# Kernel optimization log

Measured on AMD Instinct MI355X. Metric: run time of the kernel, lower is better.

Reference implementation:

```python
import jax, jax.numpy as jnp
import numpy as np

B, C, H, W = 64, 64, 64, 64
KD = 64  # kernel_dim == res == dim (required by the torch reshapes)


def _ln(t, g, b, eps=1e-5):
    mu = jnp.mean(t, axis=-1, keepdims=True)
    var = jnp.var(t, axis=-1, keepdims=True)
    return (t - mu) * jax.lax.rsqrt(var + eps) * g + b


def _cos_map(n, kd):
    i = jnp.arange(n, dtype=jnp.float32)[:, None]
    j = jnp.arange(kd, dtype=jnp.float32)[None, :]
    return jnp.cos(i * j * jnp.pi / n) / kd


def setup_inputs() -> dict:
    key = jax.random.key(0)
    ks = jax.random.split(key, 6)
    s = 0.02
    return {
        "x": jax.random.normal(ks[0], (B, C, H, W), jnp.float32),
        "freq_embed": jax.random.normal(ks[1], (H, W, C), jnp.float32),
        "g_k": jnp.ones((C,), jnp.float32), "b_k": jnp.zeros((C,), jnp.float32),
        "Wk": jax.random.normal(ks[2], (C, KD), jnp.float32) * s, "bk": jnp.zeros((KD,), jnp.float32),
        "g_z": jnp.ones((C,), jnp.float32), "b_z": jnp.zeros((C,), jnp.float32),
        "Wz": jax.random.normal(ks[3], (C, C), jnp.float32) * s, "bz": jnp.zeros((C,), jnp.float32),
        "g_o": jnp.ones((KD,), jnp.float32), "b_o": jnp.zeros((KD,), jnp.float32),
        "Wo": jax.random.normal(ks[4], (KD, C), jnp.float32) * s, "bo": jnp.zeros((C,), jnp.float32),
    }


def reference(x, freq_embed, g_k, b_k, Wk, bk, g_z, b_z, Wz, bz, g_o, b_o, Wo, bo):
    # x: (B,C,H,W) -> (B,H,W,C), matching the torch permute branch
    x = jnp.transpose(x, (0, 2, 3, 1))
    Bc, Hc, Wc, Cc = x.shape
    kd = Wk.shape[1]
    xin = x + freq_embed[None]                    # freq_embed broadcast over batch
    k = _ln(xin, g_k, b_k) @ Wk + bk              # (B,H,W,kd)
    z = _ln(freq_embed, g_z, b_z) @ Wz + bz       # to_k(freq_embed): (H,W,C)
    cosn = _cos_map(Hc, kd)                       # (H,kd)
    cosm = _cos_map(Wc, kd)                       # (W,kd)
    i = jnp.arange(Hc, dtype=jnp.float32)[:, None]
    j = jnp.arange(Wc, dtype=jnp.float32)[None, :]
    decay = (jnp.exp(-(i + j) / max(Hc, Wc)) / kd).astype(x.dtype)  # (H,W)
    wexp = decay[:, :, None] ** z                 # (H,W,C), decay > 0
    # separable forward DCT (two kernel-1 conv1d == two contractions)
    t = jnp.einsum('nh,bhwc->bnwc', cosn, k)
    t = jnp.einsum('mw,bnwc->bnmc', cosm, t)
    t = t * wexp[None]                            # exponential-decay spectral gate
    # separable inverse DCT
    t = jnp.einsum('nh,bnmc->bhmc', cosn, t)
    t = jnp.einsum('mw,bhmc->bhwc', cosm, t)
    out = _ln(t, g_o, b_o) * jax.nn.silu(z)[None]
    out = out @ Wo + bo
    return jnp.transpose(out, (0, 3, 1, 2))       # back to BCHW
```

## Files before the change

kernel.cpp:

```cpp
#include <hip/hip_runtime.h>


typedef __attribute__((ext_vector_type(8))) short short8;
typedef __attribute__((ext_vector_type(4))) float f32x4;
typedef __attribute__((ext_vector_type(4))) unsigned short us4;

__device__ __forceinline__ unsigned short bfhi(float f) {
    return (unsigned short)(__builtin_bit_cast(unsigned int, f) >> 16);
}
__device__ __forceinline__ float hif(float f) {
    return __builtin_bit_cast(float, __builtin_bit_cast(unsigned int, f) & 0xFFFF0000u);
}
__device__ __forceinline__ int swa(int row, int col) {
    return (row << 7) + (((col >> 3) ^ (row & 7)) << 4) + ((col & 7) << 1);
}
__device__ __forceinline__ short8 fragrd(const short* buf, int row, int kc) {
    int a = (row << 7) + ((kc ^ (row & 7)) << 4);
    return *(const short8*)((const char*)buf + a);
}
__device__ __forceinline__ f32x4 mm3(short8 ah, short8 al, short8 bh, short8 bl, f32x4 acc) {
    acc = __builtin_amdgcn_mfma_f32_16x16x32_bf16(ah, bh, acc, 0, 0, 0);
    acc = __builtin_amdgcn_mfma_f32_16x16x32_bf16(ah, bl, acc, 0, 0, 0);
    acc = __builtin_amdgcn_mfma_f32_16x16x32_bf16(al, bh, acc, 0, 0, 0);
    return acc;
}

__device__ __forceinline__ void mm_block(const short* Ah, const short* Al,
                                         const short* Bh, const short* Bl,
                                         int m0, int n0, int l15, int q,
                                         f32x4 (&acc)[2][2]) {
    const f32x4 zero = {0.f, 0.f, 0.f, 0.f};
    acc[0][0] = zero; acc[0][1] = zero; acc[1][0] = zero; acc[1][1] = zero;
    #pragma unroll
    for (int kb = 0; kb < 2; ++kb) {
        int kc = (kb << 2) + q;
        short8 a0h = fragrd(Ah, m0 + l15, kc);
        short8 a0l = fragrd(Al, m0 + l15, kc);
        short8 a1h = fragrd(Ah, m0 + 16 + l15, kc);
        short8 a1l = fragrd(Al, m0 + 16 + l15, kc);
        short8 b0h = fragrd(Bh, n0 + l15, kc);
        short8 b0l = fragrd(Bl, n0 + l15, kc);
        short8 b1h = fragrd(Bh, n0 + 16 + l15, kc);
        short8 b1l = fragrd(Bl, n0 + 16 + l15, kc);
        acc[0][0] = mm3(a0h, a0l, b0h, b0l, acc[0][0]);
        acc[0][1] = mm3(a0h, a0l, b1h, b1l, acc[0][1]);
        acc[1][0] = mm3(a1h, a1l, b0h, b0l, acc[1][0]);
        acc[1][1] = mm3(a1h, a1l, b1h, b1l, acc[1][1]);
    }
}

__device__ __forceinline__ void mm_block_regB(const short* Ah, const short* Al,
                                              const short8 (&bf)[2][2][2],
                                              int m0, int l15, int q,
                                              f32x4 (&acc)[2][2]) {
    const f32x4 zero = {0.f, 0.f, 0.f, 0.f};
    acc[0][0] = zero; acc[0][1] = zero; acc[1][0] = zero; acc[1][1] = zero;
    #pragma unroll
    for (int kb = 0; kb < 2; ++kb) {
        int kc = (kb << 2) + q;
        short8 a0h = fragrd(Ah, m0 + l15, kc);
        short8 a0l = fragrd(Al, m0 + l15, kc);
        short8 a1h = fragrd(Ah, m0 + 16 + l15, kc);
        short8 a1l = fragrd(Al, m0 + 16 + l15, kc);
        #pragma unroll
        for (int u = 0; u < 2; ++u) {
            acc[0][u] = mm3(a0h, a0l, bf[u][kb][0], bf[u][kb][1], acc[0][u]);
            acc[1][u] = mm3(a1h, a1l, bf[u][kb][0], bf[u][kb][1], acc[1][u]);
        }
    }
}

__global__ __launch_bounds__(256) void k_pre1(
    const float* __restrict__ g_k, const float* __restrict__ b_k,
    const float* __restrict__ Wk, const float* __restrict__ bk,
    const float* __restrict__ g_z, const float* __restrict__ b_z,
    const float* __restrict__ Wz, const float* __restrict__ bz,
    const float* __restrict__ Wo,
    unsigned short* __restrict__ WkTh, unsigned short* __restrict__ WkTl,
    float* __restrict__ su_k, float* __restrict__ v_k,
    unsigned short* __restrict__ WzTh, unsigned short* __restrict__ WzTl,
    float* __restrict__ su_z, float* __restrict__ v_z,
    unsigned short* __restrict__ WoTh, unsigned short* __restrict__ WoTl,
    unsigned short* __restrict__ cos_hi, unsigned short* __restrict__ cos_lo) {
    int t = threadIdx.x;
    if (blockIdx.x < 16) {
        int n = blockIdx.x * 4 + (t >> 6);
        int c = t & 63;
        float wk = Wk[c * 64 + n];
        float a = g_k[c] * wk;
        WkTh[n * 64 + c] = bfhi(a);
        WkTl[n * 64 + c] = bfhi(a - hif(a));
        float sa = a, sv = b_k[c] * wk;
        #pragma unroll
        for (int off = 32; off > 0; off >>= 1) {
            sa += __shfl_xor(sa, off, 64);
            sv += __shfl_xor(sv, off, 64);
        }
        if (c == 0) { su_k[n] = sa; v_k[n] = sv + bk[n]; }
        float wz = Wz[c * 64 + n];
        float az = g_z[c] * wz;
        WzTh[n * 64 + c] = bfhi(az);
        WzTl[n * 64 + c] = bfhi(az - hif(az));
        float saz = az, svz = b_z[c] * wz;
        #pragma unroll
        for (int off = 32; off > 0; off >>= 1) {
            saz += __shfl_xor(saz, off, 64);
            svz += __shfl_xor(svz, off, 64);
        }
        if (c == 0) { su_z[n] = saz; v_z[n] = svz + bz[n]; }
        float wo = Wo[c * 64 + n];
        WoTh[n * 64 + c] = bfhi(wo);
        WoTl[n * 64 + c] = bfhi(wo - hif(wo));
    } else {
        int idx = (blockIdx.x - 16) * 256 + t;
        int i = idx >> 6, j = idx & 63;
        float ang = (float)(i * j) * 3.14159265358979323846f * (1.0f / 64.0f);
        float v = cosf(ang) * (1.0f / 64.0f);
        cos_hi[idx] = bfhi(v);
        cos_lo[idx] = bfhi(v - hif(v));
    }
}

__global__ __launch_bounds__(256) void k_pre2(
    const float* __restrict__ freq,
    const unsigned short* __restrict__ WzTh_g, const unsigned short* __restrict__ WzTl_g,
    const float* __restrict__ su_z, const float* __restrict__ v_z,
    float* __restrict__ siluzT, float* __restrict__ wexpT,
    float* __restrict__ freqT) {
    __shared__ __align__(16) short Ah[4096], Al[4096], Bh[4096], Bl[4096];
    __shared__ float muS[64], rsS[64];
    __shared__ float tile[64][65];
    int t = threadIdx.x;
    if (blockIdx.x < 64) {
        int h = blockIdx.x;
        #pragma unroll
        for (int p = 0; p < 2; ++p) {
            int e = t + p * 256;
            int row = e >> 3, ch = e & 7;
            int a = (row << 7) + (((ch ^ (row & 7)) << 4));
            *(uint4*)((char*)Bh + a) = *(const uint4*)&WzTh_g[row * 64 + ch * 8];
            *(uint4*)((char*)Bl + a) = *(const uint4*)&WzTl_g[row * 64 + ch * 8];
        }
        int w = t >> 2, c0 = (t & 3) << 4;
        float4 fr[4];
        float s1 = 0.f, s2 = 0.f;
        #pragma unroll
        for (int i = 0; i < 4; ++i) {
            fr[i] = *(const float4*)&freq[(h * 64 + w) * 64 + c0 + 4 * i];
            s1 += fr[i].x + fr[i].y + fr[i].z + fr[i].w;
            s2 += fr[i].x * fr[i].x + fr[i].y * fr[i].y + fr[i].z * fr[i].z + fr[i].w * fr[i].w;
        }
        s1 += __shfl_xor(s1, 1, 64); s1 += __shfl_xor(s1, 2, 64);
        s2 += __shfl_xor(s2, 1, 64); s2 += __shfl_xor(s2, 2, 64);
        float mu = s1 * (1.0f / 64.0f);
        float var = s2 * (1.0f / 64.0f) - mu * mu;
        float rs = rsqrtf(var + 1e-5f);
        if ((t & 3) == 0) { muS[w] = mu; rsS[w] = rs; }
        const float* fp = (const float*)fr;
        #pragma unroll
        for (int i = 0; i < 4; ++i) {
            us4 hv, lv;
            #pragma unroll
            for (int r = 0; r < 4; ++r) {
                float f = fp[i * 4 + r];
                hv[r] = bfhi(f);
                lv[r] = bfhi(f - hif(f));
            }
            int a = swa(w, c0 + 4 * i);
            *(us4*)((char*)Ah + a) = hv;
            *(us4*)((char*)Al + a) = lv;
        }
        __syncthreads();
        int lane = t & 63, wv = t >> 6;
        int q = lane >> 4, l15 = lane & 15;
        int m0 = (wv & 1) << 5, n0 = (wv >> 1) << 5;
        f32x4 acc[2][2];
        mm_block(Ah, Al, Bh, Bl, m0, n0, l15, q, acc);
        #pragma unroll
        for (int u = 0; u < 2; ++u) {
            int c = n0 + (u << 4) + l15;
            float suc = su_z[c], vc = v_z[c];
            #pragma unroll
            for (int ti = 0; ti < 2; ++ti) {
                int wb = m0 + (ti << 4) + (q << 2);
                float4 mu4 = *(const float4*)&muS[wb];
                float4 rs4 = *(const float4*)&rsS[wb];
                float4 sil, wx;
                #pragma unroll
                for (int r = 0; r < 4; ++r) {
                    float z = ((const float*)&rs4)[r] * (acc[ti][u][r] - ((const float*)&mu4)[r] * suc) + vc;
                    float lnd = -(float)(h + wb + r) * 0.015625f - 4.1588830833596718565f;
                    ((float*)&sil)[r] = z / (1.0f + expf(-z));
                    ((float*)&wx)[r] = expf(z * lnd);
                }
                int base = (c * 64 + h) * 64 + wb;
                *(float4*)&siluzT[base] = sil;
                *(float4*)&wexpT[base] = wx;
            }
        }
    } else {
        int h = blockIdx.x - 64;
        int w = t >> 2, c0 = (t & 3) << 4;
        #pragma unroll
        for (int i = 0; i < 4; ++i)
            *(float4*)&tile[w][c0 + 4 * i] = *(const float4*)&freq[(h * 64 + w) * 64 + c0 + 4 * i];
        __syncthreads();
        int w0 = (t & 15) << 2;
        #pragma unroll
        for (int p = 0; p < 4; ++p) {
            int c = (t >> 4) + 16 * p;
            float4 fv = make_float4(tile[w0][c], tile[w0 + 1][c], tile[w0 + 2][c], tile[w0 + 3][c]);
            *(float4*)&freqT[(c * 64 + h) * 64 + w0] = fv;
        }
    }
}

__global__ __launch_bounds__(256, 4) void k_k(
    const float* __restrict__ x, const float* __restrict__ freqT,
    const unsigned short* __restrict__ WkTh_g, const unsigned short* __restrict__ WkTl_g,
    const float* __restrict__ su_k, const float* __restrict__ v_k,
    float* __restrict__ planes) {
    __shared__ __align__(16) short Ah[4096], Al[4096];
    __shared__ __align__(16) float red1[4][64], red2[4][64];
    __shared__ __align__(16) float muS[64], rsS[64];
    int b = blockIdx.x >> 6, h = blockIdx.x & 63;
    int t = threadIdx.x;
    int lane = t & 63, wv = t >> 6;
    int q = lane >> 4, l15 = lane & 15;
    int m0 = (wv & 1) << 5, n0 = (wv >> 1) << 5;
    short8 bf[2][2][2];
    #pragma unroll
    for (int u = 0; u < 2; ++u)
        #pragma unroll
        for (int kb = 0; kb < 2; ++kb) {
            int off = (n0 + (u << 4) + l15) * 64 + ((kb << 2) + q) * 8;
            bf[u][kb][0] = *(const short8*)&WkTh_g[off];
            bf[u][kb][1] = *(const short8*)&WkTl_g[off];
        }
    int g = t >> 4, w0 = (t & 15) << 2, c0 = g << 2;
    const float* xb = x + (size_t)b * 262144 + h * 64;
    float4 xv[4], fv[4];
    #pragma unroll
    for (int i = 0; i < 4; ++i) {
        xv[i] = *(const float4*)&xb[(c0 + i) * 4096 + w0];
        fv[i] = *(const float4*)&freqT[(c0 + i) * 4096 + h * 64 + w0];
    }
    float4 s1 = {0, 0, 0, 0}, s2 = {0, 0, 0, 0};
    #pragma unroll
    for (int i = 0; i < 4; ++i) {
        xv[i].x += fv[i].x; xv[i].y += fv[i].y; xv[i].z += fv[i].z; xv[i].w += fv[i].w;
        s1.x += xv[i].x; s1.y += xv[i].y; s1.z += xv[i].z; s1.w += xv[i].w;
        s2.x += xv[i].x * xv[i].x; s2.y += xv[i].y * xv[i].y;
        s2.z += xv[i].z * xv[i].z; s2.w += xv[i].w * xv[i].w;
    }
    const float* vp = (const float*)xv;
    #pragma unroll
    for (int j = 0; j < 4; ++j) {
        us4 hv, lv;
        #pragma unroll
        for (int r = 0; r < 4; ++r) {
            float f = vp[r * 4 + j];
            hv[r] = bfhi(f);
            lv[r] = bfhi(f - hif(f));
        }
        int a = swa(w0 + j, c0);
        *(us4*)((char*)Ah + a) = hv;
        *(us4*)((char*)Al + a) = lv;
    }
    #pragma unroll
    for (int r = 0; r < 4; ++r) {
        float a1 = ((const float*)&s1)[r];
        float a2 = ((const float*)&s2)[r];
        a1 += __shfl_xor(a1, 16, 64); a1 += __shfl_xor(a1, 32, 64);
        a2 += __shfl_xor(a2, 16, 64); a2 += __shfl_xor(a2, 32, 64);
        ((float*)&s1)[r] = a1;
        ((float*)&s2)[r] = a2;
    }
    if (lane < 16) {
        *(float4*)&red1[wv][lane << 2] = s1;
        *(float4*)&red2[wv][lane << 2] = s2;
    }
    __syncthreads();
    if (t < 64) {
        float a1 = red1[0][t] + red1[1][t] + red1[2][t] + red1[3][t];
        float a2 = red2[0][t] + red2[1][t] + red2[2][t] + red2[3][t];
        float mu = a1 * (1.0f / 64.0f);
        float var = a2 * (1.0f / 64.0f) - mu * mu;
        muS[t] = mu; rsS[t] = rsqrtf(var + 1e-5f);
    }
    __syncthreads();
    f32x4 acc[2][2];
    mm_block_regB(Ah, Al, bf, m0, l15, q, acc);
    #pragma unroll
    for (int u = 0; u < 2; ++u) {
        int n = n0 + (u << 4) + l15;
        float sun = su_k[n], vn = v_k[n];
        #pragma unroll
        for (int ti = 0; ti < 2; ++ti) {
            int wb = m0 + (ti << 4) + (q << 2);
            float4 mu4 = *(const float4*)&muS[wb];
            float4 rs4 = *(const float4*)&rsS[wb];
            float4 o;
            o.x = rs4.x * (acc[ti][u][0] - mu4.x * sun) + vn;
            o.y = rs4.y * (acc[ti][u][1] - mu4.y * sun) + vn;
            o.z = rs4.z * (acc[ti][u][2] - mu4.z * sun) + vn;
            o.w = rs4.w * (acc[ti][u][3] - mu4.w * sun) + vn;
            *(float4*)&planes[((size_t)(b * 64 + n) * 64 + h) * 64 + wb] = o;
        }
    }
}

__global__ __launch_bounds__(128, 2) void k_spec(
    float* __restrict__ planes,
    const unsigned short* __restrict__ cos_hi, const unsigned short* __restrict__ cos_lo,
    const float* __restrict__ wexpT) {
    __shared__ __align__(16) short DhS[2][4096], DlS[2][4096];
    int t = threadIdx.x;
    int wv = t >> 6, lane = t & 63;
    int q = lane >> 4, l15 = lane & 15;
    int pid = blockIdx.x * 2 + wv;
    int c = pid & 63;
    float* po = planes + (size_t)pid * 4096;
    const float* wx = wexpT + (size_t)c * 4096;
    short* dh = DhS[wv];
    short* dl = DlS[wv];

    short8 cf[4][2][2];
    #pragma unroll
    for (int rg = 0; rg < 4; ++rg)
        #pragma unroll
        for (int kb = 0; kb < 2; ++kb) {
            int off = (rg * 16 + l15) * 64 + ((kb << 2) + q) * 8;
            cf[rg][kb][0] = *(const short8*)&cos_hi[off];
            cf[rg][kb][1] = *(const short8*)&cos_lo[off];
        }

    #pragma unroll
    for (int jg = 0; jg < 16; ++jg) {
        float f0 = po[(jg * 4 + 0) * 64 + lane];
        float f1 = po[(jg * 4 + 1) * 64 + lane];
        float f2 = po[(jg * 4 + 2) * 64 + lane];
        float f3 = po[(jg * 4 + 3) * 64 + lane];
        us4 hv, lv;
        hv[0] = bfhi(f0); lv[0] = bfhi(f0 - hif(f0));
        hv[1] = bfhi(f1); lv[1] = bfhi(f1 - hif(f1));
        hv[2] = bfhi(f2); lv[2] = bfhi(f2 - hif(f2));
        hv[3] = bfhi(f3); lv[3] = bfhi(f3 - hif(f3));
        int a = swa(lane, jg << 2);
        *(us4*)((char*)dh + a) = hv;
        *(us4*)((char*)dl + a) = lv;
    }

    short8 af[4][2][2];
    f32x4 acc[2][2];
    const f32x4 zacc = {0.f, 0.f, 0.f, 0.f};

#define LOAD_AF()                                                            \
    _Pragma("unroll")                                                        \
    for (int rg = 0; rg < 4; ++rg) {                                         \
        _Pragma("unroll")                                                    \
        for (int kb = 0; kb < 2; ++kb) {                                     \
            af[rg][kb][0] = fragrd(dh, rg * 16 + l15, (kb << 2) + q);        \
            af[rg][kb][1] = fragrd(dl, rg * 16 + l15, (kb << 2) + q);        \
        }                                                                    \
    }

#define QMM(ASRC, BSRC)                                                      \
    acc[0][0] = zacc; acc[0][1] = zacc; acc[1][0] = zacc; acc[1][1] = zacc;  \
    __builtin_amdgcn_s_setprio(1);                                           \
    _Pragma("unroll")                                                        \
    for (int kb = 0; kb < 2; ++kb)                                           \
        _Pragma("unroll")                                                    \
        for (int ti = 0; ti < 2; ++ti)                                       \
            _Pragma("unroll")                                                \
            for (int u = 0; u < 2; ++u)                                      \
                acc[ti][u] = mm3(ASRC[2 * mq + ti][kb][0], ASRC[2 * mq + ti][kb][1], \
                                 BSRC[2 * nq + u][kb][0], BSRC[2 * nq + u][kb][1],   \
                                 acc[ti][u]);                                \
    __builtin_amdgcn_s_setprio(0);

#define WB_T()                                                               \
    _Pragma("unroll")                                                        \
    for (int ti = 0; ti < 2; ++ti)                                           \
        _Pragma("unroll")                                                    \
        for (int u = 0; u < 2; ++u) {                                        \
            int row = (nq << 5) + (u << 4) + l15;                            \
            int col = (mq << 5) + (ti << 4) + (q << 2);                      \
            int a = swa(row, col);                                           \
            us4 hv, lv;                                                      \
            _Pragma("unroll")                                                \
            for (int r = 0; r < 4; ++r) {                                    \
                float f = acc[ti][u][r];                                     \
                hv[r] = bfhi(f);                                             \
                lv[r] = bfhi(f - hif(f));                                    \
            }                                                                \
            *(us4*)((char*)dh + a) = hv;                                     \
            *(us4*)((char*)dl + a) = lv;                                     \
        }

    LOAD_AF()
    #pragma unroll
    for (int mq = 0; mq < 2; ++mq)
        #pragma unroll
        for (int nq = 0; nq < 2; ++nq) {
            QMM(af, cf)
            WB_T()
        }

    LOAD_AF()
    #pragma unroll
    for (int mq = 0; mq < 2; ++mq)
        #pragma unroll
        for (int nq = 0; nq < 2; ++nq) {
            float wxr[2][2][4];
            #pragma unroll
            for (int ti = 0; ti < 2; ++ti)
                #pragma unroll
                for (int u = 0; u < 2; ++u)
                    #pragma unroll
                    for (int r = 0; r < 4; ++r)
                        wxr[ti][u][r] = wx[((mq << 5) + (ti << 4) + (q << 2) + r) * 64
                                           + (nq << 5) + (u << 4) + l15];
            QMM(af, cf)
            #pragma unroll
            for (int ti = 0; ti < 2; ++ti)
                #pragma unroll
                for (int u = 0; u < 2; ++u)
                    #pragma unroll
                    for (int r = 0; r < 4; ++r)
                        acc[ti][u][r] *= wxr[ti][u][r];
            WB_T()
        }

    LOAD_AF()
    #pragma unroll
    for (int mq = 0; mq < 2; ++mq)
        #pragma unroll
        for (int nq = 0; nq < 2; ++nq) {
            QMM(cf, af)
            #pragma unroll
            for (int ti = 0; ti < 2; ++ti)
                #pragma unroll
                for (int u = 0; u < 2; ++u)
                    #pragma unroll
                    for (int r = 0; r < 4; ++r) {
                        int row = (mq << 5) + (ti << 4) + (q << 2) + r;
                        int col = (nq << 5) + (u << 4) + l15;
                        int a = swa(row, col);
                        float f = acc[ti][u][r];
                        *(unsigned short*)((char*)dh + a) = bfhi(f);
                        *(unsigned short*)((char*)dl + a) = bfhi(f - hif(f));
                    }
        }

    LOAD_AF()
    #pragma unroll
    for (int mq = 0; mq < 2; ++mq)
        #pragma unroll
        for (int nq = 0; nq < 2; ++nq) {
            QMM(af, cf)
            #pragma unroll
            for (int ti = 0; ti < 2; ++ti)
                #pragma unroll
                for (int u = 0; u < 2; ++u)
                    #pragma unroll
                    for (int r = 0; r < 4; ++r) {
                        int h = (mq << 5) + (ti << 4) + (q << 2) + r;
                        int w = (nq << 5) + (u << 4) + l15;
                        po[h * 64 + w] = acc[ti][u][r];
                    }
        }
#undef LOAD_AF
#undef QMM
#undef WB_T
}

__global__ __launch_bounds__(256, 4) void k_out(
    const float* __restrict__ planes, const float* __restrict__ siluzT,
    const float* __restrict__ g_o, const float* __restrict__ b_o,
    const unsigned short* __restrict__ WoTh_g, const unsigned short* __restrict__ WoTl_g,
    const float* __restrict__ bo, float* __restrict__ out) {
    __shared__ __align__(16) short Ah[4096], Al[4096];
    __shared__ __align__(16) float red1[4][64], red2[4][64];
    __shared__ __align__(16) float muS[64], rsS[64];
    int b = blockIdx.x >> 6, h = blockIdx.x & 63;
    int t = threadIdx.x;
    int lane = t & 63, wv = t >> 6;
    int q = lane >> 4, l15 = lane & 15;
    int m0 = (wv & 1) << 5, n0 = (wv >> 1) << 5;
    short8 bf[2][2][2];
    #pragma unroll
    for (int u = 0; u < 2; ++u)
        #pragma unroll
        for (int kb = 0; kb < 2; ++kb) {
            int off = (n0 + (u << 4) + l15) * 64 + ((kb << 2) + q) * 8;
            bf[u][kb][0] = *(const short8*)&WoTh_g[off];
            bf[u][kb][1] = *(const short8*)&WoTl_g[off];
        }
    int g = t >> 4, w0 = (t & 15) << 2, c0 = g << 2;
    const float* pb = planes + (size_t)b * 262144 + h * 64;
    float4 vr[4], szr[4];
    #pragma unroll
    for (int i = 0; i < 4; ++i) {
        vr[i] = *(const float4*)&pb[(c0 + i) * 4096 + w0];
        szr[i] = *(const float4*)&siluzT[(c0 + i) * 4096 + h * 64 + w0];
    }
    float4 s1 = {0, 0, 0, 0}, s2 = {0, 0, 0, 0};
    #pragma unroll
    for (int i = 0; i < 4; ++i) {
        s1.x += vr[i].x; s1.y += vr[i].y; s1.z += vr[i].z; s1.w += vr[i].w;
        s2.x += vr[i].x * vr[i].x; s2.y += vr[i].y * vr[i].y;
        s2.z += vr[i].z * vr[i].z; s2.w += vr[i].w * vr[i].w;
    }
    #pragma unroll
    for (int r = 0; r < 4; ++r) {
        float a1 = ((const float*)&s1)[r];
        float a2 = ((const float*)&s2)[r];
        a1 += __shfl_xor(a1, 16, 64); a1 += __shfl_xor(a1, 32, 64);
        a2 += __shfl_xor(a2, 16, 64); a2 += __shfl_xor(a2, 32, 64);
        ((float*)&s1)[r] = a1;
        ((float*)&s2)[r] = a2;
    }
    if (lane < 16) {
        *(float4*)&red1[wv][lane << 2] = s1;
        *(float4*)&red2[wv][lane << 2] = s2;
    }
    __syncthreads();
    if (t < 64) {
        float a1 = red1[0][t] + red1[1][t] + red1[2][t] + red1[3][t];
        float a2 = red2[0][t] + red2[1][t] + red2[2][t] + red2[3][t];
        float mu = a1 * (1.0f / 64.0f);
        float var = a2 * (1.0f / 64.0f) - mu * mu;
        muS[t] = mu; rsS[t] = rsqrtf(var + 1e-5f);
    }
    __syncthreads();
    {
        float4 mu4 = *(const float4*)&muS[w0];
        float4 rs4 = *(const float4*)&rsS[w0];
        #pragma unroll
        for (int i = 0; i < 4; ++i) {
            int cc = c0 + i;
            float go = g_o[cc], boc = b_o[cc];
            vr[i].x = ((vr[i].x - mu4.x) * rs4.x * go + boc) * szr[i].x;
            vr[i].y = ((vr[i].y - mu4.y) * rs4.y * go + boc) * szr[i].y;
            vr[i].z = ((vr[i].z - mu4.z) * rs4.z * go + boc) * szr[i].z;
            vr[i].w = ((vr[i].w - mu4.w) * rs4.w * go + boc) * szr[i].w;
        }
        const float* vp = (const float*)vr;
        #pragma unroll
        for (int j = 0; j < 4; ++j) {
            us4 hv, lv;
            #pragma unroll
            for (int r = 0; r < 4; ++r) {
                float f = vp[r * 4 + j];
                hv[r] = bfhi(f);
                lv[r] = bfhi(f - hif(f));
            }
            int a = swa(w0 + j, c0);
            *(us4*)((char*)Ah + a) = hv;
            *(us4*)((char*)Al + a) = lv;
        }
    }
    __syncthreads();
    f32x4 acc[2][2];
    mm_block_regB(Ah, Al, bf, m0, l15, q, acc);
    #pragma unroll
    for (int u = 0; u < 2; ++u) {
        int o_ = n0 + (u << 4) + l15;
        float bov = bo[o_];
        #pragma unroll
        for (int ti = 0; ti < 2; ++ti) {
            int wb = m0 + (ti << 4) + (q << 2);
            float4 o;
            o.x = acc[ti][u][0] + bov;
            o.y = acc[ti][u][1] + bov;
            o.z = acc[ti][u][2] + bov;
            o.w = acc[ti][u][3] + bov;
            *(float4*)&out[((size_t)(b * 64 + o_) * 64 + h) * 64 + wb] = o;
        }
    }
}

extern "C" void kernel_launch(void* const* d_in, const int* in_sizes, int n_in,
                              void* d_out, int out_size, void* d_ws, size_t ws_size,
                              hipStream_t stream) {
    const float* x    = (const float*)d_in[0];
    const float* freq = (const float*)d_in[1];
    const float* g_k  = (const float*)d_in[2];
    const float* b_k  = (const float*)d_in[3];
    const float* Wk   = (const float*)d_in[4];
    const float* bk   = (const float*)d_in[5];
    const float* g_z  = (const float*)d_in[6];
    const float* b_z  = (const float*)d_in[7];
    const float* Wz   = (const float*)d_in[8];
    const float* bz   = (const float*)d_in[9];
    const float* g_o  = (const float*)d_in[10];
    const float* b_o  = (const float*)d_in[11];
    const float* Wo   = (const float*)d_in[12];
    const float* bo   = (const float*)d_in[13];
    float* out = (float*)d_out;

    float* ws = (float*)d_ws;
    float* planes = ws;
    float* siluzT = planes + 16777216;
    float* wexpT  = siluzT + 262144;
    float* freqT  = wexpT + 262144;
    float* su_k   = freqT + 262144;
    float* v_k    = su_k + 64;
    float* su_z   = v_k + 64;
    float* v_z    = su_z + 64;
    unsigned short* cos_hi = (unsigned short*)(v_z + 64);
    unsigned short* cos_lo = cos_hi + 4096;
    unsigned short* WkTh = cos_lo + 4096;
    unsigned short* WkTl = WkTh + 4096;
    unsigned short* WzTh = WkTl + 4096;
    unsigned short* WzTl = WzTh + 4096;
    unsigned short* WoTh = WzTl + 4096;
    unsigned short* WoTl = WoTh + 4096;

    k_pre1<<<32, 256, 0, stream>>>(g_k, b_k, Wk, bk, g_z, b_z, Wz, bz, Wo,
                                   WkTh, WkTl, su_k, v_k, WzTh, WzTl, su_z, v_z,
                                   WoTh, WoTl, cos_hi, cos_lo);
    k_pre2<<<128, 256, 0, stream>>>(freq, WzTh, WzTl, su_z, v_z, siluzT, wexpT, freqT);
    k_k<<<4096, 256, 0, stream>>>(x, freqT, WkTh, WkTl, su_k, v_k, planes);
    k_spec<<<2048, 128, 0, stream>>>(planes, cos_hi, cos_lo, wexpT);
    k_out<<<4096, 256, 0, stream>>>(planes, siluzT, g_o, b_o, WoTh, WoTl, bo, out);
}
```

Before: 230.7 us.

## Process four rows per block in k_k/k_out with register prefetch and padded plane stride

Each block of k_k and k_out now handles four h rows instead of one. It double-buffers the shared A tiles and prefetches the next rows' global loads into registers while the current row's MFMA runs. The planes and transposed per-channel buffers get a padded stride (4160 instead of 4096), apparently to reduce channel/bank conflicts across planes. This cuts the grid size by four and amortises the weight-fragment loads, at the cost of more registers and shared memory, with launch bounds lowered to 3 blocks per CU.

```diff
diff --git a/kernel.cpp b/kernel.cpp
--- a/kernel.cpp
+++ b/kernel.cpp
@@ -1,5 +1,8 @@
 #include <hip/hip_runtime.h>
 
+
+#define PL_ST 4160
+#define TC_ST 4160
 
 typedef __attribute__((ext_vector_type(8))) short short8;
 typedef __attribute__((ext_vector_type(4))) float f32x4;
@@ -193,7 +196,7 @@
                     ((float*)&sil)[r] = z / (1.0f + expf(-z));
                     ((float*)&wx)[r] = expf(z * lnd);
                 }
-                int base = (c * 64 + h) * 64 + wb;
+                size_t base = (size_t)c * TC_ST + h * 64 + wb;
                 *(float4*)&siluzT[base] = sil;
                 *(float4*)&wexpT[base] = wx;
             }
@@ -210,20 +213,20 @@
         for (int p = 0; p < 4; ++p) {
             int c = (t >> 4) + 16 * p;
             float4 fv = make_float4(tile[w0][c], tile[w0 + 1][c], tile[w0 + 2][c], tile[w0 + 3][c]);
-            *(float4*)&freqT[(c * 64 + h) * 64 + w0] = fv;
-        }
-    }
-}
-
-__global__ __launch_bounds__(256, 4) void k_k(
+            *(float4*)&freqT[(size_t)c * TC_ST + h * 64 + w0] = fv;
+        }
+    }
+}
+
+__global__ __launch_bounds__(256, 3) void k_k(
     const float* __restrict__ x, const float* __restrict__ freqT,
     const unsigned short* __restrict__ WkTh_g, const unsigned short* __restrict__ WkTl_g,
     const float* __restrict__ su_k, const float* __restrict__ v_k,
     float* __restrict__ planes) {
-    __shared__ __align__(16) short Ah[4096], Al[4096];
+    __shared__ __align__(16) short Ah[2][4096], Al[2][4096];
     __shared__ __align__(16) float red1[4][64], red2[4][64];
-    __shared__ __align__(16) float muS[64], rsS[64];
-    int b = blockIdx.x >> 6, h = blockIdx.x & 63;
+    __shared__ float muS[64], rsS[64];
+    int b = blockIdx.x >> 4, h0 = (blockIdx.x & 15) << 2;
     int t = threadIdx.x;
     int lane = t & 63, wv = t >> 6;
     int q = lane >> 4, l15 = lane & 15;
@@ -238,74 +241,93 @@
             bf[u][kb][1] = *(const short8*)&WkTl_g[off];
         }
     int g = t >> 4, w0 = (t & 15) << 2, c0 = g << 2;
-    const float* xb = x + (size_t)b * 262144 + h * 64;
-    float4 xv[4], fv[4];
-    #pragma unroll
-    for (int i = 0; i < 4; ++i) {
-        xv[i] = *(const float4*)&xb[(c0 + i) * 4096 + w0];
-        fv[i] = *(const float4*)&freqT[(c0 + i) * 4096 + h * 64 + w0];
-    }
-    float4 s1 = {0, 0, 0, 0}, s2 = {0, 0, 0, 0};
-    #pragma unroll
-    for (int i = 0; i < 4; ++i) {
-        xv[i].x += fv[i].x; xv[i].y += fv[i].y; xv[i].z += fv[i].z; xv[i].w += fv[i].w;
-        s1.x += xv[i].x; s1.y += xv[i].y; s1.z += xv[i].z; s1.w += xv[i].w;
-        s2.x += xv[i].x * xv[i].x; s2.y += xv[i].y * xv[i].y;
-        s2.z += xv[i].z * xv[i].z; s2.w += xv[i].w * xv[i].w;
-    }
-    const float* vp = (const float*)xv;
-    #pragma unroll
-    for (int j = 0; j < 4; ++j) {
-        us4 hv, lv;
+    const float* xb = x + (size_t)b * 262144;
+    float4 xr[2][4], fr[2][4];
+    #pragma unroll
+    for (int pi = 0; pi < 2; ++pi) {
+        int h = h0 + pi;
+        #pragma unroll
+        for (int i = 0; i < 4; ++i) {
+            xr[pi][i] = *(const float4*)&xb[(c0 + i) * 4096 + h * 64 + w0];
+            fr[pi][i] = *(const float4*)&freqT[(size_t)(c0 + i) * TC_ST + h * 64 + w0];
+        }
+    }
+    #pragma unroll
+    for (int it = 0; it < 4; ++it) {
+        int s = it & 1;
+        int h = h0 + it;
+        float4 vv[4];
+        float4 s1 = {0, 0, 0, 0}, s2 = {0, 0, 0, 0};
+        #pragma unroll
+        for (int i = 0; i < 4; ++i) {
+            float4 a = xr[s][i], f = fr[s][i];
+            a.x += f.x; a.y += f.y; a.z += f.z; a.w += f.w;
+            vv[i] = a;
+            s1.x += a.x; s1.y += a.y; s1.z += a.z; s1.w += a.w;
+            s2.x += a.x * a.x; s2.y += a.y * a.y; s2.z += a.z * a.z; s2.w += a.w * a.w;
+        }
+        const float* vp = (const float*)vv;
+        #pragma unroll
+        for (int j = 0; j < 4; ++j) {
+            us4 hv, lv;
+            #pragma unroll
+            for (int r = 0; r < 4; ++r) {
+                float f = vp[r * 4 + j];
+                hv[r] = bfhi(f);
+                lv[r] = bfhi(f - hif(f));
+            }
+            int a = swa(w0 + j, c0);
+            *(us4*)((char*)Ah[s] + a) = hv;
+            *(us4*)((char*)Al[s] + a) = lv;
+        }
         #pragma unroll
         for (int r = 0; r < 4; ++r) {
-            float f = vp[r * 4 + j];
-            hv[r] = bfhi(f);
-            lv[r] = bfhi(f - hif(f));
-        }
-        int a = swa(w0 + j, c0);
-        *(us4*)((char*)Ah + a) = hv;
-        *(us4*)((char*)Al + a) = lv;
-    }
-    #pragma unroll
-    for (int r = 0; r < 4; ++r) {
-        float a1 = ((const float*)&s1)[r];
-        float a2 = ((const float*)&s2)[r];
-        a1 += __shfl_xor(a1, 16, 64); a1 += __shfl_xor(a1, 32, 64);
-        a2 += __shfl_xor(a2, 16, 64); a2 += __shfl_xor(a2, 32, 64);
-        ((float*)&s1)[r] = a1;
-        ((float*)&s2)[r] = a2;
-    }
-    if (lane < 16) {
-        *(float4*)&red1[wv][lane << 2] = s1;
-        *(float4*)&red2[wv][lane << 2] = s2;
-    }
-    __syncthreads();
-    if (t < 64) {
-        float a1 = red1[0][t] + red1[1][t] + red1[2][t] + red1[3][t];
-        float a2 = red2[0][t] + red2[1][t] + red2[2][t] + red2[3][t];
-        float mu = a1 * (1.0f / 64.0f);
-        float var = a2 * (1.0f / 64.0f) - mu * mu;
-        muS[t] = mu; rsS[t] = rsqrtf(var + 1e-5f);
-    }
-    __syncthreads();
-    f32x4 acc[2][2];
-    mm_block_regB(Ah, Al, bf, m0, l15, q, acc);
-    #pragma unroll
-    for (int u = 0; u < 2; ++u) {
-        int n = n0 + (u << 4) + l15;
-        float sun = su_k[n], vn = v_k[n];
-        #pragma unroll
-        for (int ti = 0; ti < 2; ++ti) {
-            int wb = m0 + (ti << 4) + (q << 2);
-            float4 mu4 = *(const float4*)&muS[wb];
-            float4 rs4 = *(const float4*)&rsS[wb];
-            float4 o;
-            o.x = rs4.x * (acc[ti][u][0] - mu4.x * sun) + vn;
-            o.y = rs4.y * (acc[ti][u][1] - mu4.y * sun) + vn;
-            o.z = rs4.z * (acc[ti][u][2] - mu4.z * sun) + vn;
-            o.w = rs4.w * (acc[ti][u][3] - mu4.w * sun) + vn;
-            *(float4*)&planes[((size_t)(b * 64 + n) * 64 + h) * 64 + wb] = o;
+            float a1 = ((const float*)&s1)[r];
+            float a2 = ((const float*)&s2)[r];
+            a1 += __shfl_xor(a1, 16, 64); a1 += __shfl_xor(a1, 32, 64);
+            a2 += __shfl_xor(a2, 16, 64); a2 += __shfl_xor(a2, 32, 64);
+            ((float*)&s1)[r] = a1;
+            ((float*)&s2)[r] = a2;
+        }
+        if (lane < 16) {
+            *(float4*)&red1[wv][lane << 2] = s1;
+            *(float4*)&red2[wv][lane << 2] = s2;
+        }
+        __syncthreads();
+        if (t < 64) {
+            float a1 = red1[0][t] + red1[1][t] + red1[2][t] + red1[3][t];
+            float a2 = red2[0][t] + red2[1][t] + red2[2][t] + red2[3][t];
+            float mu = a1 * (1.0f / 64.0f);
+            float var = a2 * (1.0f / 64.0f) - mu * mu;
+            muS[t] = mu; rsS[t] = rsqrtf(var + 1e-5f);
+        }
+        __syncthreads();
+        if (it < 2) {
+            int hn = h0 + it + 2;
+            #pragma unroll
+            for (int i = 0; i < 4; ++i) {
+                xr[s][i] = *(const float4*)&xb[(c0 + i) * 4096 + hn * 64 + w0];
+                fr[s][i] = *(const float4*)&freqT[(size_t)(c0 + i) * TC_ST + hn * 64 + w0];
+            }
+        }
+        f32x4 acc[2][2];
+        mm_block_regB(Ah[s], Al[s], bf, m0, l15, q, acc);
+        #pragma unroll
+        for (int u = 0; u < 2; ++u) {
+            int n = n0 + (u << 4) + l15;
+            float sun = su_k[n], vn = v_k[n];
+            #pragma unroll
+            for (int ti = 0; ti < 2; ++ti) {
+                int wb = m0 + (ti << 4) + (q << 2);
+                float4 mu4 = *(const float4*)&muS[wb];
+                float4 rs4 = *(const float4*)&rsS[wb];
+                float4 o;
+                o.x = rs4.x * (acc[ti][u][0] - mu4.x * sun) + vn;
+                o.y = rs4.y * (acc[ti][u][1] - mu4.y * sun) + vn;
+                o.z = rs4.z * (acc[ti][u][2] - mu4.z * sun) + vn;
+                o.w = rs4.w * (acc[ti][u][3] - mu4.w * sun) + vn;
+                *(float4*)&planes[(size_t)(b * 64 + n) * PL_ST + h * 64 + wb] = o;
+            }
         }
     }
 }
@@ -320,8 +342,8 @@
     int q = lane >> 4, l15 = lane & 15;
     int pid = blockIdx.x * 2 + wv;
     int c = pid & 63;
-    float* po = planes + (size_t)pid * 4096;
-    const float* wx = wexpT + (size_t)c * 4096;
+    float* po = planes + (size_t)pid * PL_ST;
+    const float* wx = wexpT + (size_t)c * TC_ST;
     short* dh = DhS[wv];
     short* dl = DlS[wv];
 
@@ -475,15 +497,15 @@
 #undef WB_T
 }
 
-__global__ __launch_bounds__(256, 4) void k_out(
+__global__ __launch_bounds__(256, 3) void k_out(
     const float* __restrict__ planes, const float* __restrict__ siluzT,
     const float* __restrict__ g_o, const float* __restrict__ b_o,
     const unsigned short* __restrict__ WoTh_g, const unsigned short* __restrict__ WoTl_g,
     const float* __restrict__ bo, float* __restrict__ out) {
-    __shared__ __align__(16) short Ah[4096], Al[4096];
+    __shared__ __align__(16) short Ah[2][4096], Al[2][4096];
     __shared__ __align__(16) float red1[4][64], red2[4][64];
-    __shared__ __align__(16) float muS[64], rsS[64];
-    int b = blockIdx.x >> 6, h = blockIdx.x & 63;
+    __shared__ float muS[64], rsS[64];
+    int b = blockIdx.x >> 4, h0 = (blockIdx.x & 15) << 2;
     int t = threadIdx.x;
     int lane = t & 63, wv = t >> 6;
     int q = lane >> 4, l15 = lane & 15;
@@ -498,85 +520,104 @@
             bf[u][kb][1] = *(const short8*)&WoTl_g[off];
         }
     int g = t >> 4, w0 = (t & 15) << 2, c0 = g << 2;
-    const float* pb = planes + (size_t)b * 262144 + h * 64;
-    float4 vr[4], szr[4];
-    #pragma unroll
-    for (int i = 0; i < 4; ++i) {
-        vr[i] = *(const float4*)&pb[(c0 + i) * 4096 + w0];
-        szr[i] = *(const float4*)&siluzT[(c0 + i) * 4096 + h * 64 + w0];
-    }
-    float4 s1 = {0, 0, 0, 0}, s2 = {0, 0, 0, 0};
-    #pragma unroll
-    for (int i = 0; i < 4; ++i) {
-        s1.x += vr[i].x; s1.y += vr[i].y; s1.z += vr[i].z; s1.w += vr[i].w;
-        s2.x += vr[i].x * vr[i].x; s2.y += vr[i].y * vr[i].y;
-        s2.z += vr[i].z * vr[i].z; s2.w += vr[i].w * vr[i].w;
-    }
-    #pragma unroll
-    for (int r = 0; r < 4; ++r) {
-        float a1 = ((const float*)&s1)[r];
-        float a2 = ((const float*)&s2)[r];
-        a1 += __shfl_xor(a1, 16, 64); a1 += __shfl_xor(a1, 32, 64);
-        a2 += __shfl_xor(a2, 16, 64); a2 += __shfl_xor(a2, 32, 64);
-        ((float*)&s1)[r] = a1;
-        ((float*)&s2)[r] = a2;
-    }
-    if (lane < 16) {
-        *(float4*)&red1[wv][lane << 2] = s1;
-        *(float4*)&red2[wv][lane << 2] = s2;
-    }
-    __syncthreads();
-    if (t < 64) {
-        float a1 = red1[0][t] + red1[1][t] + red1[2][t] + red1[3][t];
-        float a2 = red2[0][t] + red2[1][t] + red2[2][t] + red2[3][t];
-        float mu = a1 * (1.0f / 64.0f);
-        float var = a2 * (1.0f / 64.0f) - mu * mu;
-        muS[t] = mu; rsS[t] = rsqrtf(var + 1e-5f);
-    }
-    __syncthreads();
-    {
-        float4 mu4 = *(const float4*)&muS[w0];
-        float4 rs4 = *(const float4*)&rsS[w0];
+    float4 pr[2][4], sz[2][4];
+    #pragma unroll
+    for (int pi = 0; pi < 2; ++pi) {
+        int h = h0 + pi;
         #pragma unroll
         for (int i = 0; i < 4; ++i) {
-            int cc = c0 + i;
-            float go = g_o[cc], boc = b_o[cc];
-            vr[i].x = ((vr[i].x - mu4.x) * rs4.x * go + boc) * szr[i].x;
-            vr[i].y = ((vr[i].y - mu4.y) * rs4.y * go + boc) * szr[i].y;
-            vr[i].z = ((vr[i].z - mu4.z) * rs4.z * go + boc) * szr[i].z;
-            vr[i].w = ((vr[i].w - mu4.w) * rs4.w * go + boc) * szr[i].w;
-        }
-        const float* vp = (const float*)vr;
-        #pragma unroll
-        for (int j = 0; j < 4; ++j) {
-            us4 hv, lv;
-            #pragma unroll
-            for (int r = 0; r < 4; ++r) {
-                float f = vp[r * 4 + j];
-                hv[r] = bfhi(f);
-                lv[r] = bfhi(f - hif(f));
-            }
-            int a = swa(w0 + j, c0);
-            *(us4*)((char*)Ah + a) = hv;
-            *(us4*)((char*)Al + a) = lv;
-        }
-    }
-    __syncthreads();
-    f32x4 acc[2][2];
-    mm_block_regB(Ah, Al, bf, m0, l15, q, acc);
-    #pragma unroll
-    for (int u = 0; u < 2; ++u) {
-        int o_ = n0 + (u << 4) + l15;
-        float bov = bo[o_];
-        #pragma unroll
-        for (int ti = 0; ti < 2; ++ti) {
-            int wb = m0 + (ti << 4) + (q << 2);
-            float4 o;
-            o.x = acc[ti][u][0] + bov;
-            o.y = acc[ti][u][1] + bov;
-            o.z = acc[ti][u][2] + bov;
-            o.w = acc[ti][u][3] + bov;
-            *(float4*)&out[((size_t)(b * 64 + o_) * 64 + h) * 64 + wb] = o;
+            pr[pi][i] = *(const float4*)&planes[(size_t)(b * 64 + c0 + i) * PL_ST + h * 64 + w0];
+            sz[pi][i] = *(const float4*)&siluzT[(size_t)(c0 + i) * TC_ST + h * 64 + w0];
+        }
+    }
+    #pragma unroll
+    for (int it = 0; it < 4; ++it) {
+        int s = it & 1;
+        int h = h0 + it;
+        float4 s1 = {0, 0, 0, 0}, s2 = {0, 0, 0, 0};
+        #pragma unroll
+        for (int i = 0; i < 4; ++i) {
+            float4 tv = pr[s][i];
+            s1.x += tv.x; s1.y += tv.y; s1.z += tv.z; s1.w += tv.w;
+            s2.x += tv.x * tv.x; s2.y += tv.y * tv.y;
+            s2.z += tv.z * tv.z; s2.w += tv.w * tv.w;
+        }
+        #pragma unroll
+        for (int r = 0; r < 4; ++r) {
+            float a1 = ((const float*)&s1)[r];
+            float a2 = ((const float*)&s2)[r];
+            a1 += __shfl_xor(a1, 16, 64); a1 += __shfl_xor(a1, 32, 64);
+            a2 += __shfl_xor(a2, 16, 64); a2 += __shfl_xor(a2, 32, 64);
+            ((float*)&s1)[r] = a1;
+            ((float*)&s2)[r] = a2;
+        }
+        if (lane < 16) {
+            *(float4*)&red1[wv][lane << 2] = s1;
+            *(float4*)&red2[wv][lane << 2] = s2;
+        }
+        __syncthreads();
+        if (t < 64) {
+            float a1 = red1[0][t] + red1[1][t] + red1[2][t] + red1[3][t];
+            float a2 = red2[0][t] + red2[1][t] + red2[2][t] + red2[3][t];
+            float mu = a1 * (1.0f / 64.0f);
+            float var = a2 * (1.0f / 64.0f) - mu * mu;
+            muS[t] = mu; rsS[t] = rsqrtf(var + 1e-5f);
+        }
+        __syncthreads();
+        {
+            float4 mu4 = *(const float4*)&muS[w0];
+            float4 rs4 = *(const float4*)&rsS[w0];
+            float4 vr[4];
+            #pragma unroll
+            for (int i = 0; i < 4; ++i) {
+                int cc = c0 + i;
+                float go = g_o[cc], boc = b_o[cc];
+                float4 tv = pr[s][i], sv = sz[s][i];
+                vr[i].x = ((tv.x - mu4.x) * rs4.x * go + boc) * sv.x;
+                vr[i].y = ((tv.y - mu4.y) * rs4.y * go + boc) * sv.y;
+                vr[i].z = ((tv.z - mu4.z) * rs4.z * go + boc) * sv.z;
+                vr[i].w = ((tv.w - mu4.w) * rs4.w * go + boc) * sv.w;
+            }
+            const float* vp = (const float*)vr;
+            #pragma unroll
+            for (int j = 0; j < 4; ++j) {
+                us4 hv, lv;
+                #pragma unroll
+                for (int r = 0; r < 4; ++r) {
+                    float f = vp[r * 4 + j];
+                    hv[r] = bfhi(f);
+                    lv[r] = bfhi(f - hif(f));
+                }
+                int a = swa(w0 + j, c0);
+                *(us4*)((char*)Ah[s] + a) = hv;
+                *(us4*)((char*)Al[s] + a) = lv;
+            }
+        }
+        if (it < 2) {
+            int hn = h0 + it + 2;
+            #pragma unroll
+            for (int i = 0; i < 4; ++i) {
+                pr[s][i] = *(const float4*)&planes[(size_t)(b * 64 + c0 + i) * PL_ST + hn * 64 + w0];
+                sz[s][i] = *(const float4*)&siluzT[(size_t)(c0 + i) * TC_ST + hn * 64 + w0];
+            }
+        }
+        __syncthreads();
+        f32x4 acc[2][2];
+        mm_block_regB(Ah[s], Al[s], bf, m0, l15, q, acc);
+        #pragma unroll
+        for (int u = 0; u < 2; ++u) {
+            int o_ = n0 + (u << 4) + l15;
+            float bov = bo[o_];
+            #pragma unroll
+            for (int ti = 0; ti < 2; ++ti) {
+                int wb = m0 + (ti << 4) + (q << 2);
+                float4 o;
+                o.x = acc[ti][u][0] + bov;
+                o.y = acc[ti][u][1] + bov;
+                o.z = acc[ti][u][2] + bov;
+                o.w = acc[ti][u][3] + bov;
+                *(float4*)&out[((size_t)(b * 64 + o_) * 64 + h) * 64 + wb] = o;
+            }
         }
     }
 }
@@ -602,10 +643,10 @@
 
     float* ws = (float*)d_ws;
     float* planes = ws;
-    float* siluzT = planes + 16777216;
-    float* wexpT  = siluzT + 262144;
-    float* freqT  = wexpT + 262144;
-    float* su_k   = freqT + 262144;
+    float* siluzT = planes + (size_t)4096 * PL_ST;
+    float* wexpT  = siluzT + (size_t)64 * TC_ST;
+    float* freqT  = wexpT + (size_t)64 * TC_ST;
+    float* su_k   = freqT + (size_t)64 * TC_ST;
     float* v_k    = su_k + 64;
     float* su_z   = v_k + 64;
     float* v_z    = su_z + 64;
@@ -622,7 +663,7 @@
                                    WkTh, WkTl, su_k, v_k, WzTh, WzTl, su_z, v_z,
                                    WoTh, WoTl, cos_hi, cos_lo);
     k_pre2<<<128, 256, 0, stream>>>(freq, WzTh, WzTl, su_z, v_z, siluzT, wexpT, freqT);
-    k_k<<<4096, 256, 0, stream>>>(x, freqT, WkTh, WkTl, su_k, v_k, planes);
+    k_k<<<1024, 256, 0, stream>>>(x, freqT, WkTh, WkTl, su_k, v_k, planes);
     k_spec<<<2048, 128, 0, stream>>>(planes, cos_hi, cos_lo, wexpT);
-    k_out<<<4096, 256, 0, stream>>>(planes, siluzT, g_o, b_o, WoTh, WoTl, bo, out);
-}
+    k_out<<<1024, 256, 0, stream>>>(planes, siluzT, g_o, b_o, WoTh, WoTl, bo, out);
+}
```

Result: no change. 233.0 us (+1.0%).
